# Performance work log

Measured on AMD Instinct MI355X. Metric: run time of the kernel, lower is better.

The kernel has to match this reference:

```python
import jax, jax.numpy as jnp
import numpy as np

N_NODES = 50000
N_EDGES = 800000
NUM_GRAPHS = 256
EPS = 1e-5


def _gcn_conv(x, edge_index, W, b):
    # PyG GCNConv: add self-loops, sym-normalize, aggregate, then add bias.
    n = x.shape[0]
    xw = x @ W  # [N, out]
    loops = jnp.arange(n)
    row = jnp.concatenate([edge_index[0], loops])  # source
    col = jnp.concatenate([edge_index[1], loops])  # target
    deg = jax.ops.segment_sum(jnp.ones_like(col, dtype=xw.dtype), col, num_segments=n)
    dinv = jnp.where(deg > 0, jax.lax.rsqrt(deg), 0.0)
    norm = dinv[row] * dinv[col]  # [E+N]
    msg = norm[:, None] * xw[row]  # gather + scale
    out = jax.ops.segment_sum(msg, col, num_segments=n)  # scatter-add
    return out + b


def _bn(x, g, b, m, v):
    # inference-mode batch norm
    return (x - m) * jax.lax.rsqrt(v + EPS) * g + b


def reference(x, edge_index, batch, gcn_W0, gcn_b0, bn_g0, bn_b0, bn_m0, bn_v0,
              gcn_W1, gcn_b1, bn_g1, bn_b1, bn_m1, bn_v1,
              hW1, hb1, hg1, hbb1, hm1, hv1,
              hW2, hb2, hg2, hbb2, hm2, hv2,
              hW3, hb3, hW4, hb4):
    # GCN block 0
    h = _gcn_conv(x, edge_index, gcn_W0, gcn_b0)
    h = jax.nn.relu(_bn(h, bn_g0, bn_b0, bn_m0, bn_v0))  # dropout = identity (eval)
    # GCN block 1
    h = _gcn_conv(h, edge_index, gcn_W1, gcn_b1)
    h = jax.nn.relu(_bn(h, bn_g1, bn_b1, bn_m1, bn_v1))
    # global mean pool over graphs
    sums = jax.ops.segment_sum(h, batch, num_segments=NUM_GRAPHS)
    cnts = jax.ops.segment_sum(jnp.ones_like(batch, dtype=h.dtype), batch, num_segments=NUM_GRAPHS)
    pooled = sums / jnp.maximum(cnts, 1.0)[:, None]  # [G, 64]
    # MLP head (eval: dropout identity)
    z = jax.nn.relu(_bn(pooled @ hW1 + hb1, hg1, hbb1, hm1, hv1))
    z = jax.nn.relu(_bn(z @ hW2 + hb2, hg2, hbb2, hm2, hv2))
    z = jax.nn.relu(z @ hW3 + hb3)
    out = (z @ hW4 + hb4).reshape(-1)  # [G]
    return out


def setup_inputs() -> dict:
    key = jax.random.key(0)
    ks = jax.random.split(key, 12)
    d = 64
    inp = {
        'x': jax.random.normal(ks[0], (N_NODES, d), dtype=jnp.float32),
        'edge_index': jax.random.randint(ks[1], (2, N_EDGES), 0, N_NODES, dtype=jnp.int64),
        'batch': jnp.sort(jax.random.randint(ks[2], (N_NODES,), 0, NUM_GRAPHS, dtype=jnp.int64)),
        'gcn_W0': jax.random.normal(ks[3], (d, d), dtype=jnp.float32) * 0.1,
        'gcn_b0': jnp.zeros((d,), jnp.float32),
        'bn_g0': jnp.ones((d,), jnp.float32), 'bn_b0': jnp.zeros((d,), jnp.float32),
        'bn_m0': jnp.zeros((d,), jnp.float32), 'bn_v0': jnp.ones((d,), jnp.float32),
        'gcn_W1': jax.random.normal(ks[4], (d, d), dtype=jnp.float32) * 0.1,
        'gcn_b1': jnp.zeros((d,), jnp.float32),
        'bn_g1': jnp.ones((d,), jnp.float32), 'bn_b1': jnp.zeros((d,), jnp.float32),
        'bn_m1': jnp.zeros((d,), jnp.float32), 'bn_v1': jnp.ones((d,), jnp.float32),
        'hW1': jax.random.normal(ks[5], (d, 256), dtype=jnp.float32) * 0.1,
        'hb1': jnp.zeros((256,), jnp.float32),
        'hg1': jnp.ones((256,), jnp.float32), 'hbb1': jnp.zeros((256,), jnp.float32),
        'hm1': jnp.zeros((256,), jnp.float32), 'hv1': jnp.ones((256,), jnp.float32),
        'hW2': jax.random.normal(ks[6], (256, 128), dtype=jnp.float32) * 0.1,
        'hb2': jnp.zeros((128,), jnp.float32),
        'hg2': jnp.ones((128,), jnp.float32), 'hbb2': jnp.zeros((128,), jnp.float32),
        'hm2': jnp.zeros((128,), jnp.float32), 'hv2': jnp.ones((128,), jnp.float32),
        'hW3': jax.random.normal(ks[7], (128, 64), dtype=jnp.float32) * 0.1,
        'hb3': jnp.zeros((64,), jnp.float32),
        'hW4': jax.random.normal(ks[8], (64, 1), dtype=jnp.float32) * 0.1,
        'hb4': jnp.zeros((1,), jnp.float32),
    }
    return inp
```

## Files before the change

### kernel.cpp

```cpp
#include <hip/hip_runtime.h>
#include <hip/hip_bf16.h>
#include <hip/hip_fp16.h>

#define N_NODES 50000
#define N_EDGES 800000
#define NUM_GRAPHS 256
#define D 64
#define EPS 1e-5f
#define N_PART 8
#define PART_SIZE (N_NODES / N_PART)
#define SCAT_CHUNKS 512
#define SCAT_GRID (SCAT_CHUNKS * N_PART)
#define GEMM_BLOCKS ((N_NODES + 63) / 64)
#define WP 72

typedef _Float16 half8_t __attribute__((ext_vector_type(8)));
typedef _Float16 half4_t __attribute__((ext_vector_type(4)));
typedef float f32x4 __attribute__((ext_vector_type(4)));

__device__ __forceinline__ void acc16(const uint4& v, float w, float4& A, float4& B) {
    const __half2* hp = (const __half2*)&v;
    float2 q0 = __half22float2(hp[0]), q1 = __half22float2(hp[1]);
    float2 q2 = __half22float2(hp[2]), q3 = __half22float2(hp[3]);
    A.x += w * q0.x; A.y += w * q0.y; A.z += w * q1.x; A.w += w * q1.y;
    B.x += w * q2.x; B.y += w * q2.y; B.z += w * q3.x; B.w += w * q3.y;
}

__global__ __launch_bounds__(256) void build_gemm_kernel(
        const int* __restrict__ ei, int* __restrict__ cnt,
        unsigned short* __restrict__ ssrc, int cap,
        const float* __restrict__ X, const float* __restrict__ W,
        __half* __restrict__ Yh) {
    __shared__ _Float16 Xs[64 * WP];
    __shared__ _Float16 Wt[64 * WP];
    if (blockIdx.x >= GEMM_BLOCKS) {
        int scat  = blockIdx.x - GEMM_BLOCKS;
        int p     = blockIdx.x & (N_PART - 1);
        int chunk = scat >> 3;
        const int per = (((N_EDGES + SCAT_CHUNKS - 1) / SCAT_CHUNKS) + 3) & ~3;
        int lo = chunk * per;
        int hi = lo + per; if (hi > N_EDGES) hi = N_EDGES;
        for (int e4 = lo + (int)threadIdx.x * 4; e4 < hi; e4 += 1024) {
            int4 c4 = *(const int4*)&ei[N_EDGES + e4];
            const int* cc = (const int*)&c4;
#pragma unroll
            for (int k = 0; k < 4; k++) {
                int e = e4 + k;
                if (e < hi) {
                    int c = cc[k];
                    if (c / PART_SIZE == p) {
                        int r = ei[e];
                        int pos = atomicAdd(&cnt[c], 1);
                        if (pos < cap) ssrc[(size_t)c * cap + pos] = (unsigned short)r;
                    }
                }
            }
        }
        return;
    }
    int tid  = threadIdx.x;
    int base = blockIdx.x * 64;
    for (int i = tid; i < 4096; i += 256) {
        int k = i >> 6, n = i & 63;
        Wt[n * WP + k] = (_Float16)W[i];
    }
    for (int i = tid; i < 1024; i += 256) {
        int r = i >> 4, c4 = (i & 15) * 4;
        f32x4 xv;
        if (base + r < N_NODES) {
            xv = __builtin_nontemporal_load(
                     &((const f32x4*)X)[(size_t)(base + r) * 16 + (i & 15)]);
        } else {
            xv = (f32x4){0.f, 0.f, 0.f, 0.f};
        }
        _Float16* dst = &Xs[r * WP + c4];
        dst[0] = (_Float16)xv.x; dst[1] = (_Float16)xv.y;
        dst[2] = (_Float16)xv.z; dst[3] = (_Float16)xv.w;
    }
    __syncthreads();
    int wave  = tid >> 6;
    int lane  = tid & 63;
    int m     = lane & 15;
    int q     = lane >> 4;
    int row16 = wave * 16;
    half8_t a0 = *(const half8_t*)&Xs[(row16 + m) * WP + q * 8];
    half8_t a1 = *(const half8_t*)&Xs[(row16 + m) * WP + 32 + q * 8];
    f32x4 acc[4];
#pragma unroll
    for (int ct = 0; ct < 4; ct++) {
        half8_t b0 = *(const half8_t*)&Wt[(ct * 16 + m) * WP + q * 8];
        half8_t b1 = *(const half8_t*)&Wt[(ct * 16 + m) * WP + 32 + q * 8];
        f32x4 c = {0.f, 0.f, 0.f, 0.f};
        c = __builtin_amdgcn_mfma_f32_16x16x32_f16(a0, b0, c, 0, 0, 0);
        c = __builtin_amdgcn_mfma_f32_16x16x32_f16(a1, b1, c, 0, 0, 0);
        acc[ct] = c;
    }
#pragma unroll
    for (int ct = 0; ct < 4; ct++) {
#pragma unroll
        for (int reg = 0; reg < 4; reg++) {
            int row = base + row16 + q * 4 + reg;
            if (row < N_NODES)
                Yh[(size_t)row * 64 + ct * 16 + m] = (__half)acc[ct][reg];
        }
    }
}

template<bool OUTF16>
__global__ __launch_bounds__(256) void agg_bn_kernel(
        const __half* __restrict__ xwh, const int* __restrict__ cnt,
        const unsigned short* __restrict__ ssrc, int cap,
        const float* __restrict__ b, const float* __restrict__ g,
        const float* __restrict__ bb, const float* __restrict__ m,
        const float* __restrict__ var,
        void* __restrict__ out, int N) {
    int wave = (blockIdx.x * blockDim.x + threadIdx.x) >> 6;
    int lane = threadIdx.x & 63;
    if (wave >= N) return;
    int c   = wave;
    int sub = lane >> 3;
    int f2  = lane & 7;
    const uint4* xw8 = (const uint4*)xwh;
    int n = cnt[c];
    if (n > cap) n = cap;
    float dc = rsqrtf((float)n + 1.0f);
    size_t sbase = (size_t)c * cap;
    int idx = (lane < cap) ? (int)ssrc[sbase + lane] : 0;
    uint4 vself = make_uint4(0u, 0u, 0u, 0u);
    if (sub == 0) vself = xw8[(size_t)c * 8 + f2];
    int t = (n + 7) >> 3;
    float4 accA = make_float4(0.f, 0.f, 0.f, 0.f);
    float4 accB = accA;

    uint4 v0 = make_uint4(0u,0u,0u,0u), v1 = v0;
    int   cv0 = -1, cv1 = -1;
    auto issue = [&](int k, uint4& v, int& cv) {
        int s = k * 8 + sub;
        int sc = (s < n) ? s : 0;
        int r  = __shfl(idx, sc, 64);
        if (s >= n) r = c;
        cv = (s < n) ? cnt[r] : -1;
        v  = xw8[(size_t)r * 8 + f2];
    };
    auto consume = [&](const uint4& v, int cv) {
        if (cv >= 0) acc16(v, rsqrtf((float)cv + 1.0f), accA, accB);
    };
    if (t > 0) issue(0, v0, cv0);
    if (t > 1) issue(1, v1, cv1);
    for (int k = 0; k < t; k++) {
        consume(v0, cv0);
        v0 = v1; cv0 = cv1;
        if (k + 2 < t) issue(k + 2, v1, cv1); else cv1 = -1;
    }
    if (sub == 0) acc16(vself, dc, accA, accB);
#pragma unroll
    for (int off = 8; off < 64; off <<= 1) {
        accA.x += __shfl_xor(accA.x, off, 64); accA.y += __shfl_xor(accA.y, off, 64);
        accA.z += __shfl_xor(accA.z, off, 64); accA.w += __shfl_xor(accA.w, off, 64);
        accB.x += __shfl_xor(accB.x, off, 64); accB.y += __shfl_xor(accB.y, off, 64);
        accB.z += __shfl_xor(accB.z, off, 64); accB.w += __shfl_xor(accB.w, off, 64);
    }
    if (sub < 2) {
        int i4 = 2 * f2 + sub;
        float4 acc = sub ? accB : accA;
        float4 b4  = ((const float4*)b)[i4];
        float4 m4  = ((const float4*)m)[i4];
        float4 v4_ = ((const float4*)var)[i4];
        float4 g4  = ((const float4*)g)[i4];
        float4 bb4 = ((const float4*)bb)[i4];
        float4 h;
        h.x = (acc.x * dc + b4.x - m4.x) * (1.0f / sqrtf(v4_.x + EPS)) * g4.x + bb4.x;
        h.y = (acc.y * dc + b4.y - m4.y) * (1.0f / sqrtf(v4_.y + EPS)) * g4.y + bb4.y;
        h.z = (acc.z * dc + b4.z - m4.z) * (1.0f / sqrtf(v4_.z + EPS)) * g4.z + bb4.z;
        h.w = (acc.w * dc + b4.w - m4.w) * (1.0f / sqrtf(v4_.w + EPS)) * g4.w + bb4.w;
        h.x = h.x > 0.f ? h.x : 0.f;
        h.y = h.y > 0.f ? h.y : 0.f;
        h.z = h.z > 0.f ? h.z : 0.f;
        h.w = h.w > 0.f ? h.w : 0.f;
        if (OUTF16) {
            half4_t hv = {(_Float16)h.x, (_Float16)h.y, (_Float16)h.z, (_Float16)h.w};
            *(half4_t*)((__half*)out + (size_t)c * 64 + i4 * 4) = hv;
        } else {
            ((float4*)out)[(size_t)c * 16 + i4] = h;
        }
    }
}

__global__ __launch_bounds__(256) void gemm64h_kernel(const __half* __restrict__ Xh,
                                                      const float* __restrict__ W,
                                                      __half* __restrict__ Yh, int N) {
    __shared__ _Float16 Xs[64 * WP];
    __shared__ _Float16 Wt[64 * WP];
    int tid  = threadIdx.x;
    int base = blockIdx.x * 64;
    for (int i = tid; i < 4096; i += 256) {
        int k = i >> 6, n = i & 63;
        Wt[n * WP + k] = (_Float16)W[i];
    }
    for (int i = tid; i < 512; i += 256) {
        int r = i >> 3, c8 = (i & 7) * 8;
        uint4 v = (base + r < N)
            ? ((const uint4*)Xh)[(size_t)(base + r) * 8 + (i & 7)]
            : make_uint4(0u, 0u, 0u, 0u);
        *(uint4*)&Xs[r * WP + c8] = v;
    }
    __syncthreads();
    int wave  = tid >> 6;
    int lane  = tid & 63;
    int m     = lane & 15;
    int q     = lane >> 4;
    int row16 = wave * 16;
    half8_t a0 = *(const half8_t*)&Xs[(row16 + m) * WP + q * 8];
    half8_t a1 = *(const half8_t*)&Xs[(row16 + m) * WP + 32 + q * 8];
    f32x4 acc[4];
#pragma unroll
    for (int ct = 0; ct < 4; ct++) {
        half8_t b0 = *(const half8_t*)&Wt[(ct * 16 + m) * WP + q * 8];
        half8_t b1 = *(const half8_t*)&Wt[(ct * 16 + m) * WP + 32 + q * 8];
        f32x4 c = {0.f, 0.f, 0.f, 0.f};
        c = __builtin_amdgcn_mfma_f32_16x16x32_f16(a0, b0, c, 0, 0, 0);
        c = __builtin_amdgcn_mfma_f32_16x16x32_f16(a1, b1, c, 0, 0, 0);
        acc[ct] = c;
    }
#pragma unroll
    for (int ct = 0; ct < 4; ct++) {
#pragma unroll
        for (int reg = 0; reg < 4; reg++) {
            int row = base + row16 + q * 4 + reg;
            if (row < N)
                Yh[(size_t)row * 64 + ct * 16 + m] = (__half)acc[ct][reg];
        }
    }
}

__global__ __launch_bounds__(256) void pool_head_kernel(
        const float* __restrict__ h, const int* __restrict__ batch,
        const float* __restrict__ hW1, const float* __restrict__ hb1,
        const float* __restrict__ hg1, const float* __restrict__ hbb1,
        const float* __restrict__ hm1, const float* __restrict__ hv1,
        const float* __restrict__ hW2, const float* __restrict__ hb2,
        const float* __restrict__ hg2, const float* __restrict__ hbb2,
        const float* __restrict__ hm2, const float* __restrict__ hv2,
        const float* __restrict__ hW3, const float* __restrict__ hb3,
        const float* __restrict__ hW4, const float* __restrict__ hb4,
        float* __restrict__ out) {
    __shared__ int se[2];
    __shared__ float red[256];
    __shared__ float pooled[64];
    __shared__ float z1[256];
    __shared__ float z2[128];
    __shared__ float z3[64];
    int g = blockIdx.x;
    int t = threadIdx.x;
    if (t < 2) {
        int target = g + t;
        int lo = 0, hi = N_NODES;
        while (lo < hi) {
            int mid = (lo + hi) >> 1;
            if (batch[mid] < target) lo = mid + 1; else hi = mid;
        }
        se[t] = lo;
    }
    __syncthreads();
    int start = se[0], end = se[1];
    {
        int f = t & 63, rg = t >> 6;
        float part = 0.0f;
        for (int r = start + rg; r < end; r += 4) part += h[(size_t)r * 64 + f];
        red[t] = part;
        __syncthreads();
        if (t < 64) {
            float s = red[t] + red[t + 64] + red[t + 128] + red[t + 192];
            float cnt = (float)(end - start);
            cnt = cnt > 1.0f ? cnt : 1.0f;
            pooled[t] = s / cnt;
        }
    }
    __syncthreads();
    {
        float acc = hb1[t];
#pragma unroll
        for (int k = 0; k < 64; k++) acc += pooled[k] * hW1[k * 256 + t];
        acc = (acc - hm1[t]) * (1.0f / sqrtf(hv1[t] + EPS)) * hg1[t] + hbb1[t];
        z1[t] = acc > 0.0f ? acc : 0.0f;
    }
    __syncthreads();
    if (t < 128) {
        float acc = hb2[t];
#pragma unroll 8
        for (int k = 0; k < 256; k++) acc += z1[k] * hW2[k * 128 + t];
        acc = (acc - hm2[t]) * (1.0f / sqrtf(hv2[t] + EPS)) * hg2[t] + hbb2[t];
        z2[t] = acc > 0.0f ? acc : 0.0f;
    }
    __syncthreads();
    if (t < 64) {
        float acc = hb3[t];
#pragma unroll 8
        for (int k = 0; k < 128; k++) acc += z2[k] * hW3[k * 64 + t];
        z3[t] = acc > 0.0f ? acc : 0.0f;
    }
    __syncthreads();
    if (t < 64) {
        float v = z3[t] * hW4[t];
        for (int off = 32; off > 0; off >>= 1) v += __shfl_down(v, off, 64);
        if (t == 0) out[g] = v + hb4[0];
    }
}

extern "C" void kernel_launch(void* const* d_in, const int* in_sizes, int n_in,
                              void* d_out, int out_size, void* d_ws, size_t ws_size,
                              hipStream_t stream) {
    const float* x     = (const float*)d_in[0];
    const int*   ei    = (const int*)d_in[1];
    const int*   batch = (const int*)d_in[2];
    const float* W0 = (const float*)d_in[3];
    const float* b0 = (const float*)d_in[4];
    const float* g0 = (const float*)d_in[5];
    const float* bb0 = (const float*)d_in[6];
    const float* m0 = (const float*)d_in[7];
    const float* v0 = (const float*)d_in[8];
    const float* W1 = (const float*)d_in[9];
    const float* b1 = (const float*)d_in[10];
    const float* g1 = (const float*)d_in[11];
    const float* bb1 = (const float*)d_in[12];
    const float* m1 = (const float*)d_in[13];
    const float* v1 = (const float*)d_in[14];
    const float* hW1 = (const float*)d_in[15];
    const float* hb1 = (const float*)d_in[16];
    const float* hg1 = (const float*)d_in[17];
    const float* hbb1 = (const float*)d_in[18];
    const float* hm1 = (const float*)d_in[19];
    const float* hv1 = (const float*)d_in[20];
    const float* hW2 = (const float*)d_in[21];
    const float* hb2 = (const float*)d_in[22];
    const float* hg2 = (const float*)d_in[23];
    const float* hbb2 = (const float*)d_in[24];
    const float* hm2 = (const float*)d_in[25];
    const float* hv2 = (const float*)d_in[26];
    const float* hW3 = (const float*)d_in[27];
    const float* hb3 = (const float*)d_in[28];
    const float* hW4 = (const float*)d_in[29];
    const float* hb4 = (const float*)d_in[30];
    float* out = (float*)d_out;

    __half* xwhA = (__half*)d_ws;
    __half* xwhB = xwhA + (size_t)N_NODES * D;
    float*  bufB = (float*)(xwhB + (size_t)N_NODES * D);
    int*    cnt  = (int*)(bufB + (size_t)N_NODES * D);
    unsigned short* ssrc = (unsigned short*)(cnt + N_NODES);

    size_t used = (size_t)2 * N_NODES * D * 2 + (size_t)N_NODES * D * 4
                + (size_t)N_NODES * 4;
    int cap = 64;
    if (ws_size >= used) {
        size_t avail = (ws_size - used) / ((size_t)N_NODES * 2);
        if (avail < (size_t)cap) cap = (int)avail & ~7;
    } else {
        cap = 0;
    }

    const int NT = 256;
    hipMemsetAsync(cnt, 0, (size_t)N_NODES * 4, stream);

    build_gemm_kernel<<<SCAT_GRID + GEMM_BLOCKS, NT, 0, stream>>>(
        ei, cnt, ssrc, cap, x, W0, xwhA);

    agg_bn_kernel<true><<<(N_NODES * 64) / NT, NT, 0, stream>>>(
        xwhA, cnt, ssrc, cap, b0, g0, bb0, m0, v0, xwhB, N_NODES);

    gemm64h_kernel<<<GEMM_BLOCKS, NT, 0, stream>>>(xwhB, W1, xwhA, N_NODES);

    agg_bn_kernel<false><<<(N_NODES * 64) / NT, NT, 0, stream>>>(
        xwhA, cnt, ssrc, cap, b1, g1, bb1, m1, v1, bufB, N_NODES);

    pool_head_kernel<<<NUM_GRAPHS, NT, 0, stream>>>(bufB, batch,
        hW1, hb1, hg1, hbb1, hm1, hv1,
        hW2, hb2, hg2, hbb2, hm2, hv2,
        hW3, hb3, hW4, hb4, out);
}
```

Before: 258.2 us.

## Fuse all stages into one persistent cooperative kernel with grid syncs

```diff
diff --git a/kernel.cpp b/kernel.cpp
--- a/kernel.cpp
+++ b/kernel.cpp
@@ -1,6 +1,8 @@
 #include <hip/hip_runtime.h>
-#include <hip/hip_bf16.h>
 #include <hip/hip_fp16.h>
+#include <hip/hip_cooperative_groups.h>
+
+namespace cg = cooperative_groups;
 
 #define N_NODES 50000
 #define N_EDGES 800000
@@ -13,10 +15,25 @@
 #define SCAT_GRID (SCAT_CHUNKS * N_PART)
 #define GEMM_BLOCKS ((N_NODES + 63) / 64)
 #define WP 72
+#define MEGA_GRID 1024
 
 typedef _Float16 half8_t __attribute__((ext_vector_type(8)));
 typedef _Float16 half4_t __attribute__((ext_vector_type(4)));
 typedef float f32x4 __attribute__((ext_vector_type(4)));
+
+struct GParams {
+    const int* ei; const float* x; const int* batch;
+    const float *W0,*b0,*g0,*bb0,*m0,*v0;
+    const float *W1,*b1,*g1,*bb1,*m1,*v1;
+    const float *hW1,*hb1,*hg1,*hbb1,*hm1,*hv1;
+    const float *hW2,*hb2,*hg2,*hbb2,*hm2,*hv2;
+    const float *hW3,*hb3,*hW4,*hb4;
+    __half* xwhA;
+    __half* xwhB;
+    float*  bufB;
+    int* cnt; unsigned short* ssrc;
+    float* out; int cap;
+};
 
 __device__ __forceinline__ void acc16(const uint4& v, float w, float4& A, float4& B) {
     const __half2* hp = (const __half2*)&v;
@@ -26,50 +43,43 @@
     B.x += w * q2.x; B.y += w * q2.y; B.z += w * q3.x; B.w += w * q3.y;
 }
 
-__global__ __launch_bounds__(256) void build_gemm_kernel(
-        const int* __restrict__ ei, int* __restrict__ cnt,
-        unsigned short* __restrict__ ssrc, int cap,
-        const float* __restrict__ X, const float* __restrict__ W,
-        __half* __restrict__ Yh) {
-    __shared__ _Float16 Xs[64 * WP];
-    __shared__ _Float16 Wt[64 * WP];
-    if (blockIdx.x >= GEMM_BLOCKS) {
-        int scat  = blockIdx.x - GEMM_BLOCKS;
-        int p     = blockIdx.x & (N_PART - 1);
-        int chunk = scat >> 3;
-        const int per = (((N_EDGES + SCAT_CHUNKS - 1) / SCAT_CHUNKS) + 3) & ~3;
-        int lo = chunk * per;
-        int hi = lo + per; if (hi > N_EDGES) hi = N_EDGES;
-        for (int e4 = lo + (int)threadIdx.x * 4; e4 < hi; e4 += 1024) {
-            int4 c4 = *(const int4*)&ei[N_EDGES + e4];
-            const int* cc = (const int*)&c4;
-#pragma unroll
-            for (int k = 0; k < 4; k++) {
-                int e = e4 + k;
-                if (e < hi) {
-                    int c = cc[k];
-                    if (c / PART_SIZE == p) {
-                        int r = ei[e];
-                        int pos = atomicAdd(&cnt[c], 1);
-                        if (pos < cap) ssrc[(size_t)c * cap + pos] = (unsigned short)r;
-                    }
+__device__ __forceinline__ void scatter_chunk_dev(const GParams& P, int su) {
+    int p     = su & (N_PART - 1);
+    int chunk = su >> 3;
+    const int per = (((N_EDGES + SCAT_CHUNKS - 1) / SCAT_CHUNKS) + 3) & ~3;
+    int lo = chunk * per;
+    int hi = lo + per; if (hi > N_EDGES) hi = N_EDGES;
+    for (int e4 = lo + (int)threadIdx.x * 4; e4 < hi; e4 += 1024) {
+        int4 c4 = *(const int4*)&P.ei[N_EDGES + e4];
+        const int* cc = (const int*)&c4;
+#pragma unroll
+        for (int k = 0; k < 4; k++) {
+            int e = e4 + k;
+            if (e < hi) {
+                int c = cc[k];
+                if (c / PART_SIZE == p) {
+                    int r = P.ei[e];
+                    int pos = atomicAdd(&P.cnt[c], 1);
+                    if (pos < P.cap) P.ssrc[(size_t)c * P.cap + pos] = (unsigned short)r;
                 }
             }
         }
-        return;
-    }
-    int tid  = threadIdx.x;
-    int base = blockIdx.x * 64;
+    }
+}
+
+__device__ __forceinline__ void gemm_tile_f32in(const GParams& P, int base,
+                                                _Float16* Xs, _Float16* Wt) {
+    int tid = threadIdx.x;
     for (int i = tid; i < 4096; i += 256) {
         int k = i >> 6, n = i & 63;
-        Wt[n * WP + k] = (_Float16)W[i];
+        Wt[n * WP + k] = (_Float16)P.W0[i];
     }
     for (int i = tid; i < 1024; i += 256) {
         int r = i >> 4, c4 = (i & 15) * 4;
         f32x4 xv;
         if (base + r < N_NODES) {
             xv = __builtin_nontemporal_load(
-                     &((const f32x4*)X)[(size_t)(base + r) * 16 + (i & 15)]);
+                     &((const f32x4*)P.x)[(size_t)(base + r) * 16 + (i & 15)]);
         } else {
             xv = (f32x4){0.f, 0.f, 0.f, 0.f};
         }
@@ -78,14 +88,11 @@
         dst[2] = (_Float16)xv.z; dst[3] = (_Float16)xv.w;
     }
     __syncthreads();
-    int wave  = tid >> 6;
-    int lane  = tid & 63;
-    int m     = lane & 15;
-    int q     = lane >> 4;
+    int wave = tid >> 6, lane = tid & 63;
+    int m = lane & 15, q = lane >> 4;
     int row16 = wave * 16;
     half8_t a0 = *(const half8_t*)&Xs[(row16 + m) * WP + q * 8];
     half8_t a1 = *(const half8_t*)&Xs[(row16 + m) * WP + 32 + q * 8];
-    f32x4 acc[4];
 #pragma unroll
     for (int ct = 0; ct < 4; ct++) {
         half8_t b0 = *(const half8_t*)&Wt[(ct * 16 + m) * WP + q * 8];
@@ -93,45 +100,74 @@
         f32x4 c = {0.f, 0.f, 0.f, 0.f};
         c = __builtin_amdgcn_mfma_f32_16x16x32_f16(a0, b0, c, 0, 0, 0);
         c = __builtin_amdgcn_mfma_f32_16x16x32_f16(a1, b1, c, 0, 0, 0);
-        acc[ct] = c;
-    }
-#pragma unroll
-    for (int ct = 0; ct < 4; ct++) {
 #pragma unroll
         for (int reg = 0; reg < 4; reg++) {
             int row = base + row16 + q * 4 + reg;
             if (row < N_NODES)
-                Yh[(size_t)row * 64 + ct * 16 + m] = (__half)acc[ct][reg];
-        }
-    }
-}
-
-template<bool OUTF16>
-__global__ __launch_bounds__(256) void agg_bn_kernel(
-        const __half* __restrict__ xwh, const int* __restrict__ cnt,
-        const unsigned short* __restrict__ ssrc, int cap,
-        const float* __restrict__ b, const float* __restrict__ g,
-        const float* __restrict__ bb, const float* __restrict__ m,
-        const float* __restrict__ var,
-        void* __restrict__ out, int N) {
-    int wave = (blockIdx.x * blockDim.x + threadIdx.x) >> 6;
-    int lane = threadIdx.x & 63;
-    if (wave >= N) return;
-    int c   = wave;
+                P.xwhA[(size_t)row * 64 + ct * 16 + m] = (__half)c[reg];
+        }
+    }
+    __syncthreads();
+}
+
+__device__ __forceinline__ void gemm_tile_f16in(const GParams& P, int base,
+                                                _Float16* Xs, _Float16* Wt) {
+    int tid = threadIdx.x;
+    for (int i = tid; i < 4096; i += 256) {
+        int k = i >> 6, n = i & 63;
+        Wt[n * WP + k] = (_Float16)P.W1[i];
+    }
+    for (int i = tid; i < 512; i += 256) {
+        int r = i >> 3, c8 = (i & 7) * 8;
+        uint4 v = (base + r < N_NODES)
+            ? ((const uint4*)P.xwhB)[(size_t)(base + r) * 8 + (i & 7)]
+            : make_uint4(0u, 0u, 0u, 0u);
+        *(uint4*)&Xs[r * WP + c8] = v;
+    }
+    __syncthreads();
+    int wave = tid >> 6, lane = tid & 63;
+    int m = lane & 15, q = lane >> 4;
+    int row16 = wave * 16;
+    half8_t a0 = *(const half8_t*)&Xs[(row16 + m) * WP + q * 8];
+    half8_t a1 = *(const half8_t*)&Xs[(row16 + m) * WP + 32 + q * 8];
+#pragma unroll
+    for (int ct = 0; ct < 4; ct++) {
+        half8_t b0 = *(const half8_t*)&Wt[(ct * 16 + m) * WP + q * 8];
+        half8_t b1 = *(const half8_t*)&Wt[(ct * 16 + m) * WP + 32 + q * 8];
+        f32x4 c = {0.f, 0.f, 0.f, 0.f};
+        c = __builtin_amdgcn_mfma_f32_16x16x32_f16(a0, b0, c, 0, 0, 0);
+        c = __builtin_amdgcn_mfma_f32_16x16x32_f16(a1, b1, c, 0, 0, 0);
+#pragma unroll
+        for (int reg = 0; reg < 4; reg++) {
+            int row = base + row16 + q * 4 + reg;
+            if (row < N_NODES)
+                P.xwhA[(size_t)row * 64 + ct * 16 + m] = (__half)c[reg];
+        }
+    }
+    __syncthreads();
+}
+
+template<int MODE>
+__device__ __forceinline__ void agg_node_dev(const GParams& P, int c, int lane) {
+    const float* b   = MODE ? P.b1  : P.b0;
+    const float* g   = MODE ? P.g1  : P.g0;
+    const float* bb  = MODE ? P.bb1 : P.bb0;
+    const float* m   = MODE ? P.m1  : P.m0;
+    const float* var = MODE ? P.v1  : P.v0;
+    int cap = P.cap;
     int sub = lane >> 3;
     int f2  = lane & 7;
-    const uint4* xw8 = (const uint4*)xwh;
-    int n = cnt[c];
+    const uint4* xw8 = (const uint4*)P.xwhA;
+    int n = P.cnt[c];
     if (n > cap) n = cap;
     float dc = rsqrtf((float)n + 1.0f);
     size_t sbase = (size_t)c * cap;
-    int idx = (lane < cap) ? (int)ssrc[sbase + lane] : 0;
+    int idx = (lane < cap) ? (int)P.ssrc[sbase + lane] : 0;
     uint4 vself = make_uint4(0u, 0u, 0u, 0u);
     if (sub == 0) vself = xw8[(size_t)c * 8 + f2];
     int t = (n + 7) >> 3;
     float4 accA = make_float4(0.f, 0.f, 0.f, 0.f);
     float4 accB = accA;
-
     uint4 v0 = make_uint4(0u,0u,0u,0u), v1 = v0;
     int   cv0 = -1, cv1 = -1;
     auto issue = [&](int k, uint4& v, int& cv) {
@@ -139,7 +175,7 @@
         int sc = (s < n) ? s : 0;
         int r  = __shfl(idx, sc, 64);
         if (s >= n) r = c;
-        cv = (s < n) ? cnt[r] : -1;
+        cv = (s < n) ? P.cnt[r] : -1;
         v  = xw8[(size_t)r * 8 + f2];
     };
     auto consume = [&](const uint4& v, int cv) {
@@ -177,87 +213,29 @@
         h.y = h.y > 0.f ? h.y : 0.f;
         h.z = h.z > 0.f ? h.z : 0.f;
         h.w = h.w > 0.f ? h.w : 0.f;
-        if (OUTF16) {
+        if (MODE == 0) {
             half4_t hv = {(_Float16)h.x, (_Float16)h.y, (_Float16)h.z, (_Float16)h.w};
-            *(half4_t*)((__half*)out + (size_t)c * 64 + i4 * 4) = hv;
+            *(half4_t*)(P.xwhB + (size_t)c * 64 + i4 * 4) = hv;
         } else {
-            ((float4*)out)[(size_t)c * 16 + i4] = h;
-        }
-    }
-}
-
-__global__ __launch_bounds__(256) void gemm64h_kernel(const __half* __restrict__ Xh,
-                                                      const float* __restrict__ W,
-                                                      __half* __restrict__ Yh, int N) {
-    __shared__ _Float16 Xs[64 * WP];
-    __shared__ _Float16 Wt[64 * WP];
-    int tid  = threadIdx.x;
-    int base = blockIdx.x * 64;
-    for (int i = tid; i < 4096; i += 256) {
-        int k = i >> 6, n = i & 63;
-        Wt[n * WP + k] = (_Float16)W[i];
-    }
-    for (int i = tid; i < 512; i += 256) {
-        int r = i >> 3, c8 = (i & 7) * 8;
-        uint4 v = (base + r < N)
-            ? ((const uint4*)Xh)[(size_t)(base + r) * 8 + (i & 7)]
-            : make_uint4(0u, 0u, 0u, 0u);
-        *(uint4*)&Xs[r * WP + c8] = v;
-    }
-    __syncthreads();
-    int wave  = tid >> 6;
-    int lane  = tid & 63;
-    int m     = lane & 15;
-    int q     = lane >> 4;
-    int row16 = wave * 16;
-    half8_t a0 = *(const half8_t*)&Xs[(row16 + m) * WP + q * 8];
-    half8_t a1 = *(const half8_t*)&Xs[(row16 + m) * WP + 32 + q * 8];
-    f32x4 acc[4];
-#pragma unroll
-    for (int ct = 0; ct < 4; ct++) {
-        half8_t b0 = *(const half8_t*)&Wt[(ct * 16 + m) * WP + q * 8];
-        half8_t b1 = *(const half8_t*)&Wt[(ct * 16 + m) * WP + 32 + q * 8];
-        f32x4 c = {0.f, 0.f, 0.f, 0.f};
-        c = __builtin_amdgcn_mfma_f32_16x16x32_f16(a0, b0, c, 0, 0, 0);
-        c = __builtin_amdgcn_mfma_f32_16x16x32_f16(a1, b1, c, 0, 0, 0);
-        acc[ct] = c;
-    }
-#pragma unroll
-    for (int ct = 0; ct < 4; ct++) {
-#pragma unroll
-        for (int reg = 0; reg < 4; reg++) {
-            int row = base + row16 + q * 4 + reg;
-            if (row < N)
-                Yh[(size_t)row * 64 + ct * 16 + m] = (__half)acc[ct][reg];
-        }
-    }
-}
-
-__global__ __launch_bounds__(256) void pool_head_kernel(
-        const float* __restrict__ h, const int* __restrict__ batch,
-        const float* __restrict__ hW1, const float* __restrict__ hb1,
-        const float* __restrict__ hg1, const float* __restrict__ hbb1,
-        const float* __restrict__ hm1, const float* __restrict__ hv1,
-        const float* __restrict__ hW2, const float* __restrict__ hb2,
-        const float* __restrict__ hg2, const float* __restrict__ hbb2,
-        const float* __restrict__ hm2, const float* __restrict__ hv2,
-        const float* __restrict__ hW3, const float* __restrict__ hb3,
-        const float* __restrict__ hW4, const float* __restrict__ hb4,
-        float* __restrict__ out) {
-    __shared__ int se[2];
-    __shared__ float red[256];
-    __shared__ float pooled[64];
-    __shared__ float z1[256];
-    __shared__ float z2[128];
-    __shared__ float z3[64];
-    int g = blockIdx.x;
+            ((float4*)P.bufB)[(size_t)c * 16 + i4] = h;
+        }
+    }
+}
+
+__device__ __forceinline__ void pool_head_dev(const GParams& P, int g, float* smem) {
+    float* red    = smem;
+    float* pooled = red + 256;
+    float* z1     = pooled + 64;
+    float* z2     = z1 + 256;
+    float* z3     = z2 + 128;
+    int*   se     = (int*)(z3 + 64);
     int t = threadIdx.x;
     if (t < 2) {
         int target = g + t;
         int lo = 0, hi = N_NODES;
         while (lo < hi) {
             int mid = (lo + hi) >> 1;
-            if (batch[mid] < target) lo = mid + 1; else hi = mid;
+            if (P.batch[mid] < target) lo = mid + 1; else hi = mid;
         }
         se[t] = lo;
     }
@@ -266,7 +244,7 @@
     {
         int f = t & 63, rg = t >> 6;
         float part = 0.0f;
-        for (int r = start + rg; r < end; r += 4) part += h[(size_t)r * 64 + f];
+        for (int r = start + rg; r < end; r += 4) part += P.bufB[(size_t)r * 64 + f];
         red[t] = part;
         __syncthreads();
         if (t < 64) {
@@ -278,76 +256,114 @@
     }
     __syncthreads();
     {
-        float acc = hb1[t];
-#pragma unroll
-        for (int k = 0; k < 64; k++) acc += pooled[k] * hW1[k * 256 + t];
-        acc = (acc - hm1[t]) * (1.0f / sqrtf(hv1[t] + EPS)) * hg1[t] + hbb1[t];
+        float acc = P.hb1[t];
+#pragma unroll
+        for (int k = 0; k < 64; k++) acc += pooled[k] * P.hW1[k * 256 + t];
+        acc = (acc - P.hm1[t]) * (1.0f / sqrtf(P.hv1[t] + EPS)) * P.hg1[t] + P.hbb1[t];
         z1[t] = acc > 0.0f ? acc : 0.0f;
     }
     __syncthreads();
     if (t < 128) {
-        float acc = hb2[t];
+        float acc = P.hb2[t];
 #pragma unroll 8
-        for (int k = 0; k < 256; k++) acc += z1[k] * hW2[k * 128 + t];
-        acc = (acc - hm2[t]) * (1.0f / sqrtf(hv2[t] + EPS)) * hg2[t] + hbb2[t];
+        for (int k = 0; k < 256; k++) acc += z1[k] * P.hW2[k * 128 + t];
+        acc = (acc - P.hm2[t]) * (1.0f / sqrtf(P.hv2[t] + EPS)) * P.hg2[t] + P.hbb2[t];
         z2[t] = acc > 0.0f ? acc : 0.0f;
     }
     __syncthreads();
     if (t < 64) {
-        float acc = hb3[t];
+        float acc = P.hb3[t];
 #pragma unroll 8
-        for (int k = 0; k < 128; k++) acc += z2[k] * hW3[k * 64 + t];
+        for (int k = 0; k < 128; k++) acc += z2[k] * P.hW3[k * 64 + t];
         z3[t] = acc > 0.0f ? acc : 0.0f;
     }
     __syncthreads();
     if (t < 64) {
-        float v = z3[t] * hW4[t];
+        float v = z3[t] * P.hW4[t];
         for (int off = 32; off > 0; off >>= 1) v += __shfl_down(v, off, 64);
-        if (t == 0) out[g] = v + hb4[0];
-    }
+        if (t == 0) P.out[g] = v + P.hb4[0];
+    }
+}
+
+__global__ __launch_bounds__(256, 4) void mega_kernel(GParams P) {
+    __shared__ _Float16 Xs[64 * WP];
+    __shared__ _Float16 Wt[64 * WP];
+    cg::grid_group grid = cg::this_grid();
+    int tid = threadIdx.x, bid = blockIdx.x;
+    for (int i = bid * 256 + tid; i < N_NODES; i += MEGA_GRID * 256) P.cnt[i] = 0;
+    grid.sync();
+    for (int u = bid; u < GEMM_BLOCKS + SCAT_GRID; u += MEGA_GRID) {
+        if (u < GEMM_BLOCKS) gemm_tile_f32in(P, u * 64, Xs, Wt);
+        else                 scatter_chunk_dev(P, u - GEMM_BLOCKS);
+    }
+    grid.sync();
+    {
+        int wave = tid >> 6, lane = tid & 63;
+        for (int c = bid * 4 + wave; c < N_NODES; c += MEGA_GRID * 4)
+            agg_node_dev<0>(P, c, lane);
+    }
+    grid.sync();
+    for (int u = bid; u < GEMM_BLOCKS; u += MEGA_GRID)
+        gemm_tile_f16in(P, u * 64, Xs, Wt);
+    grid.sync();
+    {
+        int wave = tid >> 6, lane = tid & 63;
+        for (int c = bid * 4 + wave; c < N_NODES; c += MEGA_GRID * 4)
+            agg_node_dev<1>(P, c, lane);
+    }
+    grid.sync();
+    if (bid < NUM_GRAPHS) pool_head_dev(P, bid, (float*)Xs);
+}
+
+__global__ __launch_bounds__(256) void fb_build_gemm(GParams P) {
+    __shared__ _Float16 Xs[64 * WP];
+    __shared__ _Float16 Wt[64 * WP];
+    if (blockIdx.x >= GEMM_BLOCKS) scatter_chunk_dev(P, blockIdx.x - GEMM_BLOCKS);
+    else                           gemm_tile_f32in(P, blockIdx.x * 64, Xs, Wt);
+}
+template<int MODE>
+__global__ __launch_bounds__(256) void fb_agg(GParams P) {
+    int wave = (blockIdx.x * 256 + threadIdx.x) >> 6;
+    if (wave < N_NODES) agg_node_dev<MODE>(P, wave, threadIdx.x & 63);
+}
+__global__ __launch_bounds__(256) void fb_gemm1(GParams P) {
+    __shared__ _Float16 Xs[64 * WP];
+    __shared__ _Float16 Wt[64 * WP];
+    gemm_tile_f16in(P, blockIdx.x * 64, Xs, Wt);
+}
+__global__ __launch_bounds__(256) void fb_pool_head(GParams P) {
+    __shared__ float lds[772];
+    pool_head_dev(P, blockIdx.x, lds);
 }
 
 extern "C" void kernel_launch(void* const* d_in, const int* in_sizes, int n_in,
                               void* d_out, int out_size, void* d_ws, size_t ws_size,
                               hipStream_t stream) {
-    const float* x     = (const float*)d_in[0];
-    const int*   ei    = (const int*)d_in[1];
-    const int*   batch = (const int*)d_in[2];
-    const float* W0 = (const float*)d_in[3];
-    const float* b0 = (const float*)d_in[4];
-    const float* g0 = (const float*)d_in[5];
-    const float* bb0 = (const float*)d_in[6];
-    const float* m0 = (const float*)d_in[7];
-    const float* v0 = (const float*)d_in[8];
-    const float* W1 = (const float*)d_in[9];
-    const float* b1 = (const float*)d_in[10];
-    const float* g1 = (const float*)d_in[11];
-    const float* bb1 = (const float*)d_in[12];
-    const float* m1 = (const float*)d_in[13];
-    const float* v1 = (const float*)d_in[14];
-    const float* hW1 = (const float*)d_in[15];
-    const float* hb1 = (const float*)d_in[16];
-    const float* hg1 = (const float*)d_in[17];
-    const float* hbb1 = (const float*)d_in[18];
-    const float* hm1 = (const float*)d_in[19];
-    const float* hv1 = (const float*)d_in[20];
-    const float* hW2 = (const float*)d_in[21];
-    const float* hb2 = (const float*)d_in[22];
-    const float* hg2 = (const float*)d_in[23];
-    const float* hbb2 = (const float*)d_in[24];
-    const float* hm2 = (const float*)d_in[25];
-    const float* hv2 = (const float*)d_in[26];
-    const float* hW3 = (const float*)d_in[27];
-    const float* hb3 = (const float*)d_in[28];
-    const float* hW4 = (const float*)d_in[29];
-    const float* hb4 = (const float*)d_in[30];
-    float* out = (float*)d_out;
-
-    __half* xwhA = (__half*)d_ws;
-    __half* xwhB = xwhA + (size_t)N_NODES * D;
-    float*  bufB = (float*)(xwhB + (size_t)N_NODES * D);
-    int*    cnt  = (int*)(bufB + (size_t)N_NODES * D);
-    unsigned short* ssrc = (unsigned short*)(cnt + N_NODES);
+    GParams P;
+    P.ei    = (const int*)d_in[1];
+    P.x     = (const float*)d_in[0];
+    P.batch = (const int*)d_in[2];
+    P.W0 = (const float*)d_in[3];  P.b0 = (const float*)d_in[4];
+    P.g0 = (const float*)d_in[5];  P.bb0 = (const float*)d_in[6];
+    P.m0 = (const float*)d_in[7];  P.v0 = (const float*)d_in[8];
+    P.W1 = (const float*)d_in[9];  P.b1 = (const float*)d_in[10];
+    P.g1 = (const float*)d_in[11]; P.bb1 = (const float*)d_in[12];
+    P.m1 = (const float*)d_in[13]; P.v1 = (const float*)d_in[14];
+    P.hW1 = (const float*)d_in[15]; P.hb1 = (const float*)d_in[16];
+    P.hg1 = (const float*)d_in[17]; P.hbb1 = (const float*)d_in[18];
+    P.hm1 = (const float*)d_in[19]; P.hv1 = (const float*)d_in[20];
+    P.hW2 = (const float*)d_in[21]; P.hb2 = (const float*)d_in[22];
+    P.hg2 = (const float*)d_in[23]; P.hbb2 = (const float*)d_in[24];
+    P.hm2 = (const float*)d_in[25]; P.hv2 = (const float*)d_in[26];
+    P.hW3 = (const float*)d_in[27]; P.hb3 = (const float*)d_in[28];
+    P.hW4 = (const float*)d_in[29]; P.hb4 = (const float*)d_in[30];
+    P.out = (float*)d_out;
+
+    P.xwhA = (__half*)d_ws;
+    P.xwhB = P.xwhA + (size_t)N_NODES * D;
+    P.bufB = (float*)(P.xwhB + (size_t)N_NODES * D);
+    P.cnt  = (int*)(P.bufB + (size_t)N_NODES * D);
+    P.ssrc = (unsigned short*)(P.cnt + N_NODES);
 
     size_t used = (size_t)2 * N_NODES * D * 2 + (size_t)N_NODES * D * 4
                 + (size_t)N_NODES * 4;
@@ -358,23 +374,19 @@
     } else {
         cap = 0;
     }
-
-    const int NT = 256;
-    hipMemsetAsync(cnt, 0, (size_t)N_NODES * 4, stream);
-
-    build_gemm_kernel<<<SCAT_GRID + GEMM_BLOCKS, NT, 0, stream>>>(
-        ei, cnt, ssrc, cap, x, W0, xwhA);
-
-    agg_bn_kernel<true><<<(N_NODES * 64) / NT, NT, 0, stream>>>(
-        xwhA, cnt, ssrc, cap, b0, g0, bb0, m0, v0, xwhB, N_NODES);
-
-    gemm64h_kernel<<<GEMM_BLOCKS, NT, 0, stream>>>(xwhB, W1, xwhA, N_NODES);
-
-    agg_bn_kernel<false><<<(N_NODES * 64) / NT, NT, 0, stream>>>(
-        xwhA, cnt, ssrc, cap, b1, g1, bb1, m1, v1, bufB, N_NODES);
-
-    pool_head_kernel<<<NUM_GRAPHS, NT, 0, stream>>>(bufB, batch,
-        hW1, hb1, hg1, hbb1, hm1, hv1,
-        hW2, hb2, hg2, hbb2, hm2, hv2,
-        hW3, hb3, hW4, hb4, out);
-}
+    P.cap = cap;
+
+    void* kargs[] = { &P };
+    hipError_t err = hipLaunchCooperativeKernel((const void*)mega_kernel,
+                                                dim3(MEGA_GRID), dim3(256),
+                                                kargs, 0, stream);
+    if (err != hipSuccess) {
+        (void)hipGetLastError();
+        (void)hipMemsetAsync(P.cnt, 0, (size_t)N_NODES * 4, stream);
+        fb_build_gemm<<<SCAT_GRID + GEMM_BLOCKS, 256, 0, stream>>>(P);
+        fb_agg<0><<<(N_NODES * 64) / 256, 256, 0, stream>>>(P);
+        fb_gemm1<<<GEMM_BLOCKS, 256, 0, stream>>>(P);
+        fb_agg<1><<<(N_NODES * 64) / 256, 256, 0, stream>>>(P);
+        fb_pool_head<<<NUM_GRAPHS, 256, 0, stream>>>(P);
+    }
+}
```

New measurement: 913.3 us. 254% more time.
